# Optimization experiments

Hardware: AMD Instinct MI355X
Metric: run time of the kernel (lower is better)

## Reference

```python
import jax, jax.numpy as jnp
import numpy as np

S, B, D, H, E, K = 1024, 4, 1024, 16, 3, 2
DFF = 4 * D
DH = D // H


def _layernorm(x, w, b, eps=1e-5):
    mu = jnp.mean(x, axis=-1, keepdims=True)
    var = jnp.var(x, axis=-1, keepdims=True)
    return (x - mu) * jax.lax.rsqrt(var + eps) * w + b


def _quick_gelu(x):
    return x * jax.nn.sigmoid(1.702 * x)


def setup_inputs() -> dict:
    key = jax.random.key(0)
    ks = jax.random.split(key, 8)
    w = lambda k, shape: jax.random.normal(k, shape, dtype=jnp.float32) * 0.02
    return {
        "x": jax.random.normal(ks[0], (S, B, D), dtype=jnp.float32),
        "ln1_w": jnp.ones((D,), jnp.float32), "ln1_b": jnp.zeros((D,), jnp.float32),
        "ln2_w": jnp.ones((D,), jnp.float32), "ln2_b": jnp.zeros((D,), jnp.float32),
        "in_proj_w": w(ks[1], (3 * D, D)), "in_proj_b": jnp.zeros((3 * D,), jnp.float32),
        "out_proj_w": w(ks[2], (D, D)), "out_proj_b": jnp.zeros((D,), jnp.float32),
        "gate_w": w(ks[3], (E, D)),
        "fc_w": w(ks[4], (E, DFF, D)), "fc_b": jnp.zeros((E, DFF), jnp.float32),
        "proj_w": w(ks[5], (E, D, DFF)), "proj_b": jnp.zeros((E, D), jnp.float32),
    }


def _forward(x, ln1_w, ln1_b, ln2_w, ln2_b, in_proj_w, in_proj_b,
             out_proj_w, out_proj_b, gate_w, fc_w, fc_b, proj_w, proj_b):
    s, b, d = x.shape
    # --- causal self-attention (torch nn.MultiheadAttention, seq-first) ---
    h = _layernorm(x, ln1_w, ln1_b)
    qkv = h @ in_proj_w.T + in_proj_b                      # [S,B,3D]
    q, k, v = jnp.split(qkv, 3, axis=-1)
    to_bhsd = lambda t: t.reshape(s, b, H, DH).transpose(1, 2, 0, 3)  # [B,H,S,Dh]
    q, k, v = to_bhsd(q) * (DH ** -0.5), to_bhsd(k), to_bhsd(v)
    mask = jnp.where(jnp.arange(s)[:, None] >= jnp.arange(s)[None, :], 0.0, -jnp.inf)
    scores = jnp.einsum("bhqd,bhkd->bhqk", q, k) + mask    # [B,H,S,S]
    attn = jax.nn.softmax(scores, axis=-1)
    o = jnp.einsum("bhqk,bhkd->bhqd", attn, v)
    o = o.transpose(2, 0, 1, 3).reshape(s, b, d)
    x = x + (o @ out_proj_w.T + out_proj_b)

    # --- MoE routing ---
    hs = _layernorm(x, ln2_w, ln2_b)
    hs_flat = hs.reshape(-1, d)                            # [T,D], T = S*B
    router_logits = hs_flat @ gate_w.T                     # [T,E]
    rw = jax.nn.softmax(router_logits.astype(jnp.float32), axis=-1)
    top_vals, top_idx = jax.lax.top_k(rw, K)               # [T,K]
    top_vals = top_vals / jnp.sum(top_vals, axis=-1, keepdims=True)

    # dense grouped expert FFN (E=3 small, compute-all + masked combine)
    h1 = _quick_gelu(jnp.einsum("td,efd->etf", hs_flat, fc_w) + fc_b[:, None, :])
    expert_out = jnp.einsum("etf,edf->etd", h1, proj_w) + proj_b[:, None, :]  # [E,T,D]
    comb = jnp.sum(jax.nn.one_hot(top_idx, E, dtype=top_vals.dtype) * top_vals[..., None], axis=1)  # [T,E]
    final_hidden_states = jnp.einsum("te,etd->td", comb, expert_out).reshape(s, b, d)
    del final_hidden_states  # NOTE: source computes this but never uses it in the output

    gate_score = jnp.max(top_vals, axis=-1).reshape(s, b, 1)
    out = x * gate_score
    return out, router_logits


def reference(x, ln1_w, ln1_b, ln2_w, ln2_b, in_proj_w, in_proj_b,
              out_proj_w, out_proj_b, gate_w, fc_w, fc_b, proj_w, proj_b):
    return _forward(x, ln1_w, ln1_b, ln2_w, ln2_b, in_proj_w, in_proj_b,
                    out_proj_w, out_proj_b, gate_w, fc_w, fc_b, proj_w, proj_b)
```

## Files before the change

kernel.cpp:

```cpp
#include <hip/hip_runtime.h>
#include <hip/hip_bf16.h>

#define S_DIM 1024
#define B_DIM 4
#define D_DIM 1024
#define H_DIM 16
#define DH    64
#define T_DIM (S_DIM * B_DIM)
#define QKV_N (3 * D_DIM)

using bf16 = __hip_bfloat16;
typedef __attribute__((ext_vector_type(4))) float fx4;
typedef __attribute__((ext_vector_type(8))) short bx8;

__device__ __forceinline__ unsigned short f2bf(float f) {
  union { float f; unsigned int u; } cv; cv.f = f;
  unsigned int u = cv.u;
  unsigned int r = (u + 0x7FFFu + ((u >> 16) & 1u)) >> 16;
  return (unsigned short)r;
}

__device__ __forceinline__ void g2l16(const void* g, void* l) {
  __builtin_amdgcn_global_load_lds(
      (const __attribute__((address_space(1))) unsigned int*)g,
      (__attribute__((address_space(3))) unsigned int*)l, 16, 0, 0);
}

__global__ __launch_bounds__(256) void cast2_f32_bf16(
    const float* __restrict__ a, bf16* __restrict__ da, int an4,
    const float* __restrict__ b, bf16* __restrict__ db, int bn4) {
  const int i = blockIdx.x * 256 + threadIdx.x;
  const float* src; bf16* dst; int j;
  if (i < an4) { src = a; dst = da; j = i; }
  else if (i < an4 + bn4) { src = b; dst = db; j = i - an4; }
  else return;
  const fx4 v = ((const fx4*)src)[j];
  ushort4 u;
  u.x = f2bf(v[0]); u.y = f2bf(v[1]); u.z = f2bf(v[2]); u.w = f2bf(v[3]);
  ((ushort4*)dst)[j] = u;
}

__global__ __launch_bounds__(256) void ln_bf16_kernel(
    const float* __restrict__ x, const float* __restrict__ w,
    const float* __restrict__ bb, bf16* __restrict__ out) {
  const int t = blockIdx.x, tid = threadIdx.x;
  const fx4 v = ((const fx4*)(x + (size_t)t * D_DIM))[tid];
  float s  = v[0] + v[1] + v[2] + v[3];
  float ss = v[0]*v[0] + v[1]*v[1] + v[2]*v[2] + v[3]*v[3];
#pragma unroll
  for (int off = 32; off >= 1; off >>= 1) {
    s  += __shfl_xor(s, off);
    ss += __shfl_xor(ss, off);
  }
  __shared__ float red[8];
  const int wid = tid >> 6, lane = tid & 63;
  if (lane == 0) { red[wid] = s; red[4 + wid] = ss; }
  __syncthreads();
  s  = red[0] + red[1] + red[2] + red[3];
  ss = red[4] + red[5] + red[6] + red[7];
  const float mu = s * (1.f / D_DIM);
  const float rstd = rsqrtf(ss * (1.f / D_DIM) - mu * mu + 1e-5f);
  const fx4 wv = ((const fx4*)w)[tid];
  const fx4 bv = ((const fx4*)bb)[tid];
  ushort4 u;
  u.x = f2bf((v[0] - mu) * rstd * wv[0] + bv[0]);
  u.y = f2bf((v[1] - mu) * rstd * wv[1] + bv[1]);
  u.z = f2bf((v[2] - mu) * rstd * wv[2] + bv[2]);
  u.w = f2bf((v[3] - mu) * rstd * wv[3] + bv[3]);
  ((ushort4*)(out + (size_t)t * D_DIM))[tid] = u;
}

template <int EPI>
__global__ __launch_bounds__(256, 2) void gemm_bt(
    const bf16* __restrict__ A, const bf16* __restrict__ B,
    const float* __restrict__ bias, const float* __restrict__ resid,
    float* __restrict__ C, ushort* __restrict__ qkvb, int N, int K) {
  __shared__ bf16 sA[128 * 32];
  __shared__ bf16 sB[128 * 32];
  const int tid  = threadIdx.x;
  const int brow = blockIdx.y * 128;
  const int bcol = blockIdx.x * 128;
  const int wid  = tid >> 6;
  const int lane = tid & 63;
  const int wr   = wid >> 1;
  const int wc   = wid & 1;
  const int fr   = lane & 15;
  const int fk   = lane >> 4;

  fx4 acc[4][4];
#pragma unroll
  for (int i = 0; i < 4; ++i)
#pragma unroll
    for (int j = 0; j < 4; ++j) acc[i][j] = 0.f;

  const int arow = tid >> 2;
  const int acol = (tid & 3) * 8;

  for (int kt = 0; kt < K; kt += 32) {
    __syncthreads();
#pragma unroll
    for (int is = 0; is < 2; ++is) {
      const int row = is * 64 + arow;
      const int off = row * 64 + acol * 2;
      g2l16(A + (size_t)(brow + row) * K + kt + acol, (char*)sA + off);
      g2l16(B + (size_t)(bcol + row) * K + kt + acol, (char*)sB + off);
    }
    __syncthreads();

    bx8 af[4], bfr[4];
#pragma unroll
    for (int mm = 0; mm < 4; ++mm)
      af[mm] = *(const bx8*)(sA + (wr * 64 + mm * 16 + fr) * 32 + fk * 8);
#pragma unroll
    for (int nn = 0; nn < 4; ++nn)
      bfr[nn] = *(const bx8*)(sB + (wc * 64 + nn * 16 + fr) * 32 + fk * 8);
#pragma unroll
    for (int mm = 0; mm < 4; ++mm)
#pragma unroll
      for (int nn = 0; nn < 4; ++nn)
        acc[mm][nn] = __builtin_amdgcn_mfma_f32_16x16x32_bf16(
            af[mm], bfr[nn], acc[mm][nn], 0, 0, 0);
  }

  const int row0 = brow + wr * 64 + fk * 4;
  const int col0 = bcol + wc * 64 + fr;
#pragma unroll
  for (int mm = 0; mm < 4; ++mm) {
#pragma unroll
    for (int nn = 0; nn < 4; ++nn) {
      const int col = col0 + nn * 16;
      const float bv = bias[col];
      if (EPI == 1) {
#pragma unroll
        for (int rr = 0; rr < 4; ++rr) {
          const int row = row0 + mm * 16 + rr;
          C[(size_t)row * N + col] = acc[mm][nn][rr] + bv + resid[(size_t)row * N + col];
        }
      } else {
        const int which = col >> 10;
        const int rem   = col & 1023;
        const int hh    = rem >> 6;
        const int dh    = rem & 63;
        const float scale = (which == 0) ? 0.125f : 1.0f;
#pragma unroll
        for (int rr = 0; rr < 4; ++rr) {
          const int row = row0 + mm * 16 + rr;
          const int ss2 = row >> 2, bb2 = row & 3;
          const float v = (acc[mm][nn][rr] + bv) * scale;
          qkvb[(size_t)which * 4194304 +
               ((size_t)(bb2 * 16 + hh)) * 65536 + (size_t)ss2 * 64 + dh] = f2bf(v);
        }
      }
    }
  }
}

__global__ __launch_bounds__(256) void transpose_v(
    const ushort* __restrict__ v, ushort* __restrict__ vt) {
  __shared__ ushort tile[64][65];
  const int g  = blockIdx.x;
  const int bh = g >> 4, st = g & 15;
  const int s0 = st * 64;
  const int tid = threadIdx.x;
  const int r  = tid >> 2;
  const int c0 = (tid & 3) * 16;
  const ushort* src = v + (size_t)bh * 65536 + (size_t)(s0 + r) * 64 + c0;
#pragma unroll
  for (int i = 0; i < 2; ++i) {
    const bx8 d = *(const bx8*)(src + i * 8);
#pragma unroll
    for (int j = 0; j < 8; ++j) tile[r][c0 + i * 8 + j] = (ushort)d[j];
  }
  __syncthreads();
  ushort* dst = vt + (size_t)bh * 65536 + (size_t)r * 1024 + s0 + c0;
  bx8 w0, w1;
#pragma unroll
  for (int j = 0; j < 8; ++j) {
    w0[j] = (short)tile[c0 + j][r];
    w1[j] = (short)tile[c0 + 8 + j][r];
  }
  *(bx8*)dst = w0;
  *(bx8*)(dst + 8) = w1;
}

__global__ __launch_bounds__(256, 4) void attn_mfma(
    const ushort* __restrict__ qb, const ushort* __restrict__ kb,
    const ushort* __restrict__ vtb, ushort* __restrict__ ob) {
  __shared__ __align__(16) char sK[2][8192];
  __shared__ __align__(16) char sVT[2][8192];
  __shared__ __align__(16) char sP[8192];
  const int tid  = threadIdx.x;
  const int wid  = tid >> 6;
  const int lane = tid & 63;
  const int g    = blockIdx.x;
  const int bh   = g >> 3;
  const int pr   = g & 7;
  const int b    = bh >> 4, h = bh & 15;
  const int fr   = lane & 15;
  const int fk   = lane >> 4;
  const size_t bhoff = (size_t)bh * 65536;
  char* const sPw = sP + wid * 2048;
  const int swp = (fr & 7) << 4;

  auto stage = [&](int buf, int k0) {
#pragma unroll
    for (int is = 0; is < 2; ++is) {
      const int L    = is * 4096 + tid * 16;
      const int row  = L >> 7;
      const int colb = (L & 127) ^ ((row & 7) << 4);
      g2l16(kb  + bhoff + (size_t)(k0 + row) * 64 + (colb >> 1), sK[buf]  + L);
      g2l16(vtb + bhoff + (size_t)row * 1024 + k0 + (colb >> 1), sVT[buf] + L);
    }
  };

#pragma unroll 1
  for (int tile = 0; tile < 2; ++tile) {
    const int qt  = tile ? (15 - pr) : pr;
    const int q0w = qt * 64 + wid * 16;

    const ushort* qp = qb + bhoff + (size_t)(q0w + fr) * 64;
    const bx8 qf0 = *(const bx8*)(qp + fk * 8);
    const bx8 qf1 = *(const bx8*)(qp + 32 + fk * 8);

    fx4 o4[4];
    float m = -3e38f, l = 0.f;
#pragma unroll
    for (int dt = 0; dt < 4; ++dt) o4[dt] = 0.f;

    stage(0, 0);
    asm volatile("s_waitcnt vmcnt(0)" ::: "memory");
    int cur = 0;

#pragma unroll 1
    for (int kbk = 0; kbk <= qt; ++kbk) {
      if (kbk < qt) {
        stage(cur ^ 1, (kbk + 1) * 64);
        asm volatile("s_waitcnt vmcnt(4)" ::: "memory");
      } else {
        asm volatile("s_waitcnt vmcnt(0)" ::: "memory");
      }
      __builtin_amdgcn_s_barrier();
      asm volatile("" ::: "memory");
      const char* sKc  = sK[cur];
      const char* sVTc = sVT[cur];

      fx4 s4[4];
      __builtin_amdgcn_s_setprio(1);
#pragma unroll
      for (int kt = 0; kt < 4; ++kt) {
        const int krow = kt * 16 + fr;
        const int sw   = (krow & 7) << 4;
        const bx8 kf0 = *(const bx8*)(sKc + krow * 128 + ((fk * 16) ^ sw));
        const bx8 kf1 = *(const bx8*)(sKc + krow * 128 + ((64 + fk * 16) ^ sw));
        fx4 z = {0.f, 0.f, 0.f, 0.f};
        z = __builtin_amdgcn_mfma_f32_16x16x32_bf16(kf0, qf0, z, 0, 0, 0);
        s4[kt] = __builtin_amdgcn_mfma_f32_16x16x32_bf16(kf1, qf1, z, 0, 0, 0);
      }
      __builtin_amdgcn_s_setprio(0);

      if (kbk == qt) {
        const int qloc = wid * 16 + fr;
#pragma unroll
        for (int kt = 0; kt < 4; ++kt) {
          const int keyb = kt * 16 + fk * 4;
#pragma unroll
          for (int rr = 0; rr < 4; ++rr)
            if (keyb + rr > qloc) s4[kt][rr] = -3e38f;
        }
      }

      float pm = s4[0][0];
#pragma unroll
      for (int kt = 0; kt < 4; ++kt)
#pragma unroll
        for (int rr = 0; rr < 4; ++rr) pm = fmaxf(pm, s4[kt][rr]);
      pm = fmaxf(pm, __shfl_xor(pm, 16));
      pm = fmaxf(pm, __shfl_xor(pm, 32));

      if (__any(pm > m + 8.f)) {
        const float mn = fmaxf(m, pm);
        const float f  = __expf(m - mn);
        m = mn;
        l *= f;
        float fq[4];
#pragma unroll
        for (int rr = 0; rr < 4; ++rr) fq[rr] = __shfl(f, fk * 4 + rr);
#pragma unroll
        for (int dt = 0; dt < 4; ++dt)
#pragma unroll
          for (int rr = 0; rr < 4; ++rr) o4[dt][rr] *= fq[rr];
      }

#pragma unroll
      for (int kt = 0; kt < 4; ++kt) {
        const float p0 = __expf(s4[kt][0] - m);
        const float p1 = __expf(s4[kt][1] - m);
        const float p2 = __expf(s4[kt][2] - m);
        const float p3 = __expf(s4[kt][3] - m);
        l += (p0 + p1) + (p2 + p3);
        uint2 pk;
        pk.x = ((unsigned)f2bf(p0)) | (((unsigned)f2bf(p1)) << 16);
        pk.y = ((unsigned)f2bf(p2)) | (((unsigned)f2bf(p3)) << 16);
        *(uint2*)(sPw + ((fr * 128 + kt * 32 + fk * 8) ^ swp)) = pk;
      }

      __builtin_amdgcn_s_setprio(1);
#pragma unroll
      for (int c = 0; c < 2; ++c) {
        const bx8 pa = *(const bx8*)(sPw + ((fr * 128 + c * 64 + fk * 16) ^ swp));
#pragma unroll
        for (int dt = 0; dt < 4; ++dt) {
          const int vrow = dt * 16 + fr;
          const bx8 vf = *(const bx8*)(sVTc + vrow * 128 +
                                       ((c * 64 + fk * 16) ^ ((vrow & 7) << 4)));
          o4[dt] = __builtin_amdgcn_mfma_f32_16x16x32_bf16(pa, vf, o4[dt], 0, 0, 0);
        }
      }
      __builtin_amdgcn_s_setprio(0);

      asm volatile("" ::: "memory");
      __builtin_amdgcn_s_barrier();
      asm volatile("" ::: "memory");
      cur ^= 1;
    }

    l += __shfl_xor(l, 16);
    l += __shfl_xor(l, 32);
    const float linv = 1.f / l;
    float lq[4];
#pragma unroll
    for (int rr = 0; rr < 4; ++rr) lq[rr] = __shfl(linv, fk * 4 + rr);

#pragma unroll
    for (int dt = 0; dt < 4; ++dt) {
#pragma unroll
      for (int rr = 0; rr < 4; ++rr) {
        const int qq = q0w + fk * 4 + rr;
        ob[((size_t)qq * 4 + b) * 1024 + h * 64 + dt * 16 + fr] =
            f2bf(o4[dt][rr] * lq[rr]);
      }
    }
  }
}

__global__ __launch_bounds__(256) void final_kernel(
    const float* __restrict__ xn, const float* __restrict__ w,
    const float* __restrict__ bb, const float* __restrict__ gw,
    float* __restrict__ out, float* __restrict__ rlog) {
  const int t = blockIdx.x, tid = threadIdx.x;
  const fx4 v = ((const fx4*)(xn + (size_t)t * D_DIM))[tid];
  float s  = v[0] + v[1] + v[2] + v[3];
  float ss = v[0]*v[0] + v[1]*v[1] + v[2]*v[2] + v[3]*v[3];
#pragma unroll
  for (int off = 32; off >= 1; off >>= 1) {
    s  += __shfl_xor(s, off);
    ss += __shfl_xor(ss, off);
  }
  __shared__ float red[8];
  __shared__ float red2[12];
  const int wid = tid >> 6, lane = tid & 63;
  if (lane == 0) { red[wid] = s; red[4 + wid] = ss; }
  __syncthreads();
  s  = red[0] + red[1] + red[2] + red[3];
  ss = red[4] + red[5] + red[6] + red[7];
  const float mu = s * (1.f / D_DIM);
  const float rstd = rsqrtf(ss * (1.f / D_DIM) - mu * mu + 1e-5f);
  const fx4 wv = ((const fx4*)w)[tid];
  const fx4 bv = ((const fx4*)bb)[tid];
  fx4 hv;
#pragma unroll
  for (int cc = 0; cc < 4; ++cc) hv[cc] = (v[cc] - mu) * rstd * wv[cc] + bv[cc];

  const fx4 w0 = ((const fx4*)(gw           ))[tid];
  const fx4 w1 = ((const fx4*)(gw +     D_DIM))[tid];
  const fx4 w2 = ((const fx4*)(gw + 2 * D_DIM))[tid];
  float g0 = hv[0]*w0[0] + hv[1]*w0[1] + hv[2]*w0[2] + hv[3]*w0[3];
  float g1 = hv[0]*w1[0] + hv[1]*w1[1] + hv[2]*w1[2] + hv[3]*w1[3];
  float g2 = hv[0]*w2[0] + hv[1]*w2[1] + hv[2]*w2[2] + hv[3]*w2[3];
#pragma unroll
  for (int off = 32; off >= 1; off >>= 1) {
    g0 += __shfl_xor(g0, off);
    g1 += __shfl_xor(g1, off);
    g2 += __shfl_xor(g2, off);
  }
  if (lane == 0) { red2[wid] = g0; red2[4 + wid] = g1; red2[8 + wid] = g2; }
  __syncthreads();
  g0 = red2[0] + red2[1] + red2[2]  + red2[3];
  g1 = red2[4] + red2[5] + red2[6]  + red2[7];
  g2 = red2[8] + red2[9] + red2[10] + red2[11];

  const float lmax = fmaxf(g0, fmaxf(g1, g2));
  const float lmin = fminf(g0, fminf(g1, g2));
  const float lmid = (g0 + g1 + g2) - lmax - lmin;
  const float gate = 1.f / (1.f + __expf(lmid - lmax));

  ((fx4*)(out + (size_t)t * D_DIM))[tid] = v * gate;
  if (tid == 0) {
    rlog[(size_t)t * 3 + 0] = g0;
    rlog[(size_t)t * 3 + 1] = g1;
    rlog[(size_t)t * 3 + 2] = g2;
  }
}

extern "C" void kernel_launch(void* const* d_in, const int* in_sizes, int n_in,
                              void* d_out, int out_size, void* d_ws, size_t ws_size,
                              hipStream_t stream) {
  (void)in_sizes; (void)n_in; (void)out_size; (void)ws_size;
  const float* x    = (const float*)d_in[0];
  const float* ln1w = (const float*)d_in[1];
  const float* ln1b = (const float*)d_in[2];
  const float* ln2w = (const float*)d_in[3];
  const float* ln2b = (const float*)d_in[4];
  const float* win  = (const float*)d_in[5];
  const float* bin  = (const float*)d_in[6];
  const float* wout = (const float*)d_in[7];
  const float* bout = (const float*)d_in[8];
  const float* gw   = (const float*)d_in[9];

  char* ws = (char*)d_ws;
  bf16*   w_in_b  = (bf16*)(ws);
  bf16*   w_out_b = (bf16*)(ws + 6291456);
  bf16*   h_b     = (bf16*)(ws + 8388608);
  ushort* o_b     = (ushort*)h_b;
  ushort* qkvb    = (ushort*)(ws + 16777216);
  ushort* q_b     = qkvb;
  ushort* k_b     = qkvb + 4194304;
  ushort* v_b     = qkvb + 8388608;
  float*  xnew    = (float*)(ws + 41943040);
  ushort* vt_b    = (ushort*)(ws + 58720256);

  float* out  = (float*)d_out;
  float* rlog = out + (size_t)T_DIM * D_DIM;

  cast2_f32_bf16<<<4096, 256, 0, stream>>>(win, w_in_b, 786432,
                                           wout, w_out_b, 262144);
  ln_bf16_kernel<<<T_DIM, 256, 0, stream>>>(x, ln1w, ln1b, h_b);
  gemm_bt<2><<<dim3(QKV_N / 128, T_DIM / 128), 256, 0, stream>>>(
      h_b, w_in_b, bin, nullptr, nullptr, qkvb, QKV_N, D_DIM);
  transpose_v<<<1024, 256, 0, stream>>>(v_b, vt_b);
  attn_mfma<<<512, 256, 0, stream>>>(q_b, k_b, vt_b, o_b);
  gemm_bt<1><<<dim3(D_DIM / 128, T_DIM / 128), 256, 0, stream>>>(
      (const bf16*)o_b, w_out_b, bout, x, xnew, nullptr, D_DIM, D_DIM);
  final_kernel<<<T_DIM, 256, 0, stream>>>(xnew, ln2w, ln2b, gw, out, rlog);
}
```

Measured before the change: 118.5 us.

## Double-buffer GEMM LDS, exp2 softmax with truncating bf16, one q-tile per attention block

The GEMM now double-buffers its LDS tiles so the next K-slice load overlaps the MFMAs, with one barrier per iteration. Attention folds log2(e) into the Q scale so the softmax uses exp2f, packs P to bf16 by truncation instead of round-to-nearest, and raises the lazy-rescale threshold. The grid doubles to 1024 blocks, each handling one query tile, ordered longest tiles first instead of pairing short and long tiles per block. Truncating P and the larger rescale threshold change numerics slightly, and one tile per block may worsen tail balance.

Measured after the change: 115.8 us. 2.2% less time.

```diff
diff --git a/kernel.cpp b/kernel.cpp
--- a/kernel.cpp
+++ b/kernel.cpp
@@ -75,8 +75,8 @@
     const bf16* __restrict__ A, const bf16* __restrict__ B,
     const float* __restrict__ bias, const float* __restrict__ resid,
     float* __restrict__ C, ushort* __restrict__ qkvb, int N, int K) {
-  __shared__ bf16 sA[128 * 32];
-  __shared__ bf16 sB[128 * 32];
+  __shared__ bf16 sA[2][128 * 32];
+  __shared__ bf16 sB[2][128 * 32];
   const int tid  = threadIdx.x;
   const int brow = blockIdx.y * 128;
   const int bcol = blockIdx.x * 128;
@@ -96,30 +96,48 @@
   const int arow = tid >> 2;
   const int acol = (tid & 3) * 8;
 
-  for (int kt = 0; kt < K; kt += 32) {
-    __syncthreads();
+  auto stage = [&](int buf, int kt) {
 #pragma unroll
     for (int is = 0; is < 2; ++is) {
       const int row = is * 64 + arow;
       const int off = row * 64 + acol * 2;
-      g2l16(A + (size_t)(brow + row) * K + kt + acol, (char*)sA + off);
-      g2l16(B + (size_t)(bcol + row) * K + kt + acol, (char*)sB + off);
-    }
-    __syncthreads();
+      g2l16(A + (size_t)(brow + row) * K + kt + acol, (char*)sA[buf] + off);
+      g2l16(B + (size_t)(bcol + row) * K + kt + acol, (char*)sB[buf] + off);
+    }
+  };
+
+  stage(0, 0);
+  asm volatile("s_waitcnt vmcnt(0)" ::: "memory");
+  __builtin_amdgcn_s_barrier();
+  asm volatile("" ::: "memory");
+
+  const int nk = K >> 5;
+  int cur = 0;
+#pragma unroll 1
+  for (int ki = 0; ki < nk; ++ki) {
+    if (ki + 1 < nk) stage(cur ^ 1, (ki + 1) * 32);
+    asm volatile("" ::: "memory");
 
     bx8 af[4], bfr[4];
 #pragma unroll
     for (int mm = 0; mm < 4; ++mm)
-      af[mm] = *(const bx8*)(sA + (wr * 64 + mm * 16 + fr) * 32 + fk * 8);
+      af[mm] = *(const bx8*)(sA[cur] + (wr * 64 + mm * 16 + fr) * 32 + fk * 8);
 #pragma unroll
     for (int nn = 0; nn < 4; ++nn)
-      bfr[nn] = *(const bx8*)(sB + (wc * 64 + nn * 16 + fr) * 32 + fk * 8);
+      bfr[nn] = *(const bx8*)(sB[cur] + (wc * 64 + nn * 16 + fr) * 32 + fk * 8);
 #pragma unroll
     for (int mm = 0; mm < 4; ++mm)
 #pragma unroll
       for (int nn = 0; nn < 4; ++nn)
         acc[mm][nn] = __builtin_amdgcn_mfma_f32_16x16x32_bf16(
             af[mm], bfr[nn], acc[mm][nn], 0, 0, 0);
+
+    if (ki + 1 < nk) {
+      asm volatile("s_waitcnt vmcnt(0)" ::: "memory");
+      __builtin_amdgcn_s_barrier();
+      asm volatile("" ::: "memory");
+    }
+    cur ^= 1;
   }
 
   const int row0 = brow + wr * 64 + fk * 4;
@@ -141,7 +159,7 @@
         const int rem   = col & 1023;
         const int hh    = rem >> 6;
         const int dh    = rem & 63;
-        const float scale = (which == 0) ? 0.125f : 1.0f;
+        const float scale = (which == 0) ? 0.18033688f : 1.0f;
 #pragma unroll
         for (int rr = 0; rr < 4; ++rr) {
           const int row = row0 + mm * 16 + rr;
@@ -193,8 +211,8 @@
   const int wid  = tid >> 6;
   const int lane = tid & 63;
   const int g    = blockIdx.x;
-  const int bh   = g >> 3;
-  const int pr   = g & 7;
+  const int qt   = 15 - (g >> 6);
+  const int bh   = g & 63;
   const int b    = bh >> 4, h = bh & 15;
   const int fr   = lane & 15;
   const int fk   = lane >> 4;
@@ -213,132 +231,128 @@
     }
   };
 
+  const int q0w = qt * 64 + wid * 16;
+  const ushort* qp = qb + bhoff + (size_t)(q0w + fr) * 64;
+  const bx8 qf0 = *(const bx8*)(qp + fk * 8);
+  const bx8 qf1 = *(const bx8*)(qp + 32 + fk * 8);
+  asm volatile("s_waitcnt vmcnt(0)" ::: "memory");
+
+  fx4 o4[4];
+  float m = -3e38f, l = 0.f;
+#pragma unroll
+  for (int dt = 0; dt < 4; ++dt) o4[dt] = 0.f;
+
+  stage(0, 0);
+  int cur = 0;
+
 #pragma unroll 1
-  for (int tile = 0; tile < 2; ++tile) {
-    const int qt  = tile ? (15 - pr) : pr;
-    const int q0w = qt * 64 + wid * 16;
-
-    const ushort* qp = qb + bhoff + (size_t)(q0w + fr) * 64;
-    const bx8 qf0 = *(const bx8*)(qp + fk * 8);
-    const bx8 qf1 = *(const bx8*)(qp + 32 + fk * 8);
-
-    fx4 o4[4];
-    float m = -3e38f, l = 0.f;
-#pragma unroll
-    for (int dt = 0; dt < 4; ++dt) o4[dt] = 0.f;
-
-    stage(0, 0);
-    asm volatile("s_waitcnt vmcnt(0)" ::: "memory");
-    int cur = 0;
-
-#pragma unroll 1
-    for (int kbk = 0; kbk <= qt; ++kbk) {
-      if (kbk < qt) {
-        stage(cur ^ 1, (kbk + 1) * 64);
-        asm volatile("s_waitcnt vmcnt(4)" ::: "memory");
-      } else {
-        asm volatile("s_waitcnt vmcnt(0)" ::: "memory");
+  for (int kbk = 0; kbk <= qt; ++kbk) {
+    if (kbk < qt) {
+      stage(cur ^ 1, (kbk + 1) * 64);
+      asm volatile("s_waitcnt vmcnt(4)" ::: "memory");
+    } else {
+      asm volatile("s_waitcnt vmcnt(0)" ::: "memory");
+    }
+    __builtin_amdgcn_s_barrier();
+    asm volatile("" ::: "memory");
+    const char* sKc  = sK[cur];
+    const char* sVTc = sVT[cur];
+
+    fx4 s4[4];
+    __builtin_amdgcn_s_setprio(1);
+#pragma unroll
+    for (int kt = 0; kt < 4; ++kt) {
+      const int krow = kt * 16 + fr;
+      const int sw   = (krow & 7) << 4;
+      const bx8 kf0 = *(const bx8*)(sKc + krow * 128 + ((fk * 16) ^ sw));
+      const bx8 kf1 = *(const bx8*)(sKc + krow * 128 + ((64 + fk * 16) ^ sw));
+      fx4 z = {0.f, 0.f, 0.f, 0.f};
+      z = __builtin_amdgcn_mfma_f32_16x16x32_bf16(kf0, qf0, z, 0, 0, 0);
+      s4[kt] = __builtin_amdgcn_mfma_f32_16x16x32_bf16(kf1, qf1, z, 0, 0, 0);
+    }
+    __builtin_amdgcn_s_setprio(0);
+
+    if (kbk == qt) {
+      const int qloc = wid * 16 + fr;
+#pragma unroll
+      for (int kt = 0; kt < 4; ++kt) {
+        const int keyb = kt * 16 + fk * 4;
+#pragma unroll
+        for (int rr = 0; rr < 4; ++rr)
+          if (keyb + rr > qloc) s4[kt][rr] = -3e38f;
       }
-      __builtin_amdgcn_s_barrier();
-      asm volatile("" ::: "memory");
-      const char* sKc  = sK[cur];
-      const char* sVTc = sVT[cur];
-
-      fx4 s4[4];
-      __builtin_amdgcn_s_setprio(1);
-#pragma unroll
-      for (int kt = 0; kt < 4; ++kt) {
-        const int krow = kt * 16 + fr;
-        const int sw   = (krow & 7) << 4;
-        const bx8 kf0 = *(const bx8*)(sKc + krow * 128 + ((fk * 16) ^ sw));
-        const bx8 kf1 = *(const bx8*)(sKc + krow * 128 + ((64 + fk * 16) ^ sw));
-        fx4 z = {0.f, 0.f, 0.f, 0.f};
-        z = __builtin_amdgcn_mfma_f32_16x16x32_bf16(kf0, qf0, z, 0, 0, 0);
-        s4[kt] = __builtin_amdgcn_mfma_f32_16x16x32_bf16(kf1, qf1, z, 0, 0, 0);
+    }
+
+    float pm = s4[0][0];
+#pragma unroll
+    for (int kt = 0; kt < 4; ++kt)
+#pragma unroll
+      for (int rr = 0; rr < 4; ++rr) pm = fmaxf(pm, s4[kt][rr]);
+    pm = fmaxf(pm, __shfl_xor(pm, 16));
+    pm = fmaxf(pm, __shfl_xor(pm, 32));
+
+    if (__any(pm > m + 11.5f)) {
+      const float mn = fmaxf(m, pm);
+      const float f  = exp2f(m - mn);
+      m = mn;
+      l *= f;
+      float fq[4];
+#pragma unroll
+      for (int rr = 0; rr < 4; ++rr) fq[rr] = __shfl(f, fk * 4 + rr);
+#pragma unroll
+      for (int dt = 0; dt < 4; ++dt)
+#pragma unroll
+        for (int rr = 0; rr < 4; ++rr) o4[dt][rr] *= fq[rr];
+    }
+
+#pragma unroll
+    for (int kt = 0; kt < 4; ++kt) {
+      union { float f; unsigned u; } a0, a1, a2, a3;
+      a0.f = exp2f(s4[kt][0] - m);
+      a1.f = exp2f(s4[kt][1] - m);
+      a2.f = exp2f(s4[kt][2] - m);
+      a3.f = exp2f(s4[kt][3] - m);
+      l += (a0.f + a1.f) + (a2.f + a3.f);
+      uint2 pk;
+      pk.x = (a0.u >> 16) | (a1.u & 0xFFFF0000u);
+      pk.y = (a2.u >> 16) | (a3.u & 0xFFFF0000u);
+      *(uint2*)(sPw + ((fr * 128 + kt * 32 + fk * 8) ^ swp)) = pk;
+    }
+
+    __builtin_amdgcn_s_setprio(1);
+#pragma unroll
+    for (int c = 0; c < 2; ++c) {
+      const bx8 pa = *(const bx8*)(sPw + ((fr * 128 + c * 64 + fk * 16) ^ swp));
+#pragma unroll
+      for (int dt = 0; dt < 4; ++dt) {
+        const int vrow = dt * 16 + fr;
+        const bx8 vf = *(const bx8*)(sVTc + vrow * 128 +
+                                     ((c * 64 + fk * 16) ^ ((vrow & 7) << 4)));
+        o4[dt] = __builtin_amdgcn_mfma_f32_16x16x32_bf16(pa, vf, o4[dt], 0, 0, 0);
       }
-      __builtin_amdgcn_s_setprio(0);
-
-      if (kbk == qt) {
-        const int qloc = wid * 16 + fr;
-#pragma unroll
-        for (int kt = 0; kt < 4; ++kt) {
-          const int keyb = kt * 16 + fk * 4;
-#pragma unroll
-          for (int rr = 0; rr < 4; ++rr)
-            if (keyb + rr > qloc) s4[kt][rr] = -3e38f;
-        }
-      }
-
-      float pm = s4[0][0];
-#pragma unroll
-      for (int kt = 0; kt < 4; ++kt)
-#pragma unroll
-        for (int rr = 0; rr < 4; ++rr) pm = fmaxf(pm, s4[kt][rr]);
-      pm = fmaxf(pm, __shfl_xor(pm, 16));
-      pm = fmaxf(pm, __shfl_xor(pm, 32));
-
-      if (__any(pm > m + 8.f)) {
-        const float mn = fmaxf(m, pm);
-        const float f  = __expf(m - mn);
-        m = mn;
-        l *= f;
-        float fq[4];
-#pragma unroll
-        for (int rr = 0; rr < 4; ++rr) fq[rr] = __shfl(f, fk * 4 + rr);
-#pragma unroll
-        for (int dt = 0; dt < 4; ++dt)
-#pragma unroll
-          for (int rr = 0; rr < 4; ++rr) o4[dt][rr] *= fq[rr];
-      }
-
-#pragma unroll
-      for (int kt = 0; kt < 4; ++kt) {
-        const float p0 = __expf(s4[kt][0] - m);
-        const float p1 = __expf(s4[kt][1] - m);
-        const float p2 = __expf(s4[kt][2] - m);
-        const float p3 = __expf(s4[kt][3] - m);
-        l += (p0 + p1) + (p2 + p3);
-        uint2 pk;
-        pk.x = ((unsigned)f2bf(p0)) | (((unsigned)f2bf(p1)) << 16);
-        pk.y = ((unsigned)f2bf(p2)) | (((unsigned)f2bf(p3)) << 16);
-        *(uint2*)(sPw + ((fr * 128 + kt * 32 + fk * 8) ^ swp)) = pk;
-      }
-
-      __builtin_amdgcn_s_setprio(1);
-#pragma unroll
-      for (int c = 0; c < 2; ++c) {
-        const bx8 pa = *(const bx8*)(sPw + ((fr * 128 + c * 64 + fk * 16) ^ swp));
-#pragma unroll
-        for (int dt = 0; dt < 4; ++dt) {
-          const int vrow = dt * 16 + fr;
-          const bx8 vf = *(const bx8*)(sVTc + vrow * 128 +
-                                       ((c * 64 + fk * 16) ^ ((vrow & 7) << 4)));
-          o4[dt] = __builtin_amdgcn_mfma_f32_16x16x32_bf16(pa, vf, o4[dt], 0, 0, 0);
-        }
-      }
-      __builtin_amdgcn_s_setprio(0);
-
-      asm volatile("" ::: "memory");
-      __builtin_amdgcn_s_barrier();
-      asm volatile("" ::: "memory");
-      cur ^= 1;
-    }
-
-    l += __shfl_xor(l, 16);
-    l += __shfl_xor(l, 32);
-    const float linv = 1.f / l;
-    float lq[4];
-#pragma unroll
-    for (int rr = 0; rr < 4; ++rr) lq[rr] = __shfl(linv, fk * 4 + rr);
-
-#pragma unroll
-    for (int dt = 0; dt < 4; ++dt) {
-#pragma unroll
-      for (int rr = 0; rr < 4; ++rr) {
-        const int qq = q0w + fk * 4 + rr;
-        ob[((size_t)qq * 4 + b) * 1024 + h * 64 + dt * 16 + fr] =
-            f2bf(o4[dt][rr] * lq[rr]);
-      }
+    }
+    __builtin_amdgcn_s_setprio(0);
+
+    asm volatile("" ::: "memory");
+    __builtin_amdgcn_s_barrier();
+    asm volatile("" ::: "memory");
+    cur ^= 1;
+  }
+
+  l += __shfl_xor(l, 16);
+  l += __shfl_xor(l, 32);
+  const float linv = 1.f / l;
+  float lq[4];
+#pragma unroll
+  for (int rr = 0; rr < 4; ++rr) lq[rr] = __shfl(linv, fk * 4 + rr);
+
+#pragma unroll
+  for (int dt = 0; dt < 4; ++dt) {
+#pragma unroll
+    for (int rr = 0; rr < 4; ++rr) {
+      const int qq = q0w + fk * 4 + rr;
+      ob[((size_t)qq * 4 + b) * 1024 + h * 64 + dt * 16 + fr] =
+          f2bf(o4[dt][rr] * lq[rr]);
     }
   }
 }
@@ -438,7 +452,7 @@
   gemm_bt<2><<<dim3(QKV_N / 128, T_DIM / 128), 256, 0, stream>>>(
       h_b, w_in_b, bin, nullptr, nullptr, qkvb, QKV_N, D_DIM);
   transpose_v<<<1024, 256, 0, stream>>>(v_b, vt_b);
-  attn_mfma<<<512, 256, 0, stream>>>(q_b, k_b, vt_b, o_b);
+  attn_mfma<<<1024, 256, 0, stream>>>(q_b, k_b, vt_b, o_b);
   gemm_bt<1><<<dim3(D_DIM / 128, T_DIM / 128), 256, 0, stream>>>(
       (const bf16*)o_b, w_out_b, bout, x, xnew, nullptr, D_DIM, D_DIM);
   final_kernel<<<T_DIM, 256, 0, stream>>>(xnew, ln2w, ln2b, gw, out, rlog);
```
